# Optimization experiments

Measured on AMD Instinct MI355X. Metric: run time of the kernel, lower is better.

## Reference

```python
import jax, jax.numpy as jnp
import numpy as np

B, N, H, NH = 2, 2048, 1024, 16
DH = H // NH  # 64
SCALE = H ** (-0.5)  # NOTE: original scales by hidden_size**-0.5, not head_dim**-0.5


def setup_inputs() -> dict:
    key = jax.random.key(0)
    k1, k2 = jax.random.split(key)
    hidden_states = jax.random.normal(k1, (B, N, H), dtype=jnp.float32)
    attention_mask = jnp.ones((B, N), dtype=jnp.int32)
    W_qkv = jax.random.normal(k2, (3 * H, H), dtype=jnp.float32) * (H ** -0.5)
    return {"hidden_states": hidden_states, "attention_mask": attention_mask, "W_qkv": W_qkv}


def reference(hidden_states, attention_mask, W_qkv):
    b, n, _ = hidden_states.shape
    # qkv: [b, n, 3H] = x @ W^T  (torch Linear, bias=False)
    qkv = jnp.einsum('bnd,ed->bne', hidden_states, W_qkv)
    # 'b n (k h d) -> k b h n d'
    qkv = qkv.reshape(b, n, 3, NH, DH)
    q, k, v = jnp.moveaxis(qkv, 2, 0).transpose(0, 1, 3, 2, 4)  # each [b, h, n, d]
    scores = jnp.einsum('bhid,bhjd->bhij', q, k) * SCALE
    # mask-fill: attention_mask[:, None, :, None] == 0 -> masks query rows (faithful)
    mask = (attention_mask[:, None, :, None] == 0)
    scores = jnp.where(mask, jnp.asarray(-10000.0, scores.dtype), scores)
    attn = jax.nn.softmax(scores, axis=-1)
    out = jnp.einsum('bhij,bhjd->bhid', attn, v)
    # 'b h n d -> b n (h d)'
    return out.transpose(0, 2, 1, 3).reshape(b, n, NH * DH)
```

## Files before the change

### kernel.cpp

```cpp
#include <hip/hip_runtime.h>
#include <hip/hip_bf16.h>
#include <stdint.h>

#define B_ 2
#define N_ 2048
#define H_ 1024
#define NH_ 16
#define DH_ 64
#define E_ 3072
#define M_ 4096
#define K_ 1024
#define QSCALE2_ 0.0450842200277786f
#define THR2_    11.5415603f

typedef unsigned short ushort_t;
typedef short bf16x8 __attribute__((ext_vector_type(8)));
typedef float f32x4 __attribute__((ext_vector_type(4)));
typedef ushort_t ushort8 __attribute__((ext_vector_type(8)));
typedef ushort_t ushort4v __attribute__((ext_vector_type(4)));
typedef float float4v __attribute__((ext_vector_type(4)));

static __device__ __forceinline__ ushort_t f2bf(float f) {
  __hip_bfloat16 h = __float2bfloat16(f);
  ushort_t u;
  __builtin_memcpy(&u, &h, sizeof(u));
  return u;
}
static __device__ __forceinline__ uint32_t pk2bf(float lo, float hi) {
  return (uint32_t)f2bf(lo) | ((uint32_t)f2bf(hi) << 16);
}
static __device__ __forceinline__ float max3f(float a, float b, float c) {
  return fmaxf(fmaxf(a, b), c);
}

#define GLOAD_LDS16(g, l)                                                   \
  __builtin_amdgcn_global_load_lds(                                         \
      (const __attribute__((address_space(1))) void*)(g),                   \
      (__attribute__((address_space(3))) void*)(l), 16, 0, 0)

__global__ void convert_kernel(const float* __restrict__ X,
                               const float* __restrict__ W,
                               ushort_t* __restrict__ Xb,
                               ushort_t* __restrict__ Wb) {
  const int nx4 = (M_ * K_) / 4;
  int i = blockIdx.x * blockDim.x + threadIdx.x;
  if (i < nx4) {
    float4v v = ((const float4v*)X)[i];
    ushort4v o;
    o[0] = f2bf(v[0]); o[1] = f2bf(v[1]); o[2] = f2bf(v[2]); o[3] = f2bf(v[3]);
    ((ushort4v*)Xb)[i] = o;
  } else {
    int j = i - nx4;
    float4v v = ((const float4v*)W)[j];
    ushort4v o;
    o[0] = f2bf(v[0]); o[1] = f2bf(v[1]); o[2] = f2bf(v[2]); o[3] = f2bf(v[3]);
    ((ushort4v*)Wb)[j] = o;
  }
}

__global__ void gemm_qkv(const ushort_t* __restrict__ Xb,
                         const ushort_t* __restrict__ Wb,
                         ushort_t* __restrict__ Qw,
                         ushort_t* __restrict__ Kw,
                         ushort_t* __restrict__ VTw) {
  __shared__ ushort_t lds_a[128 * 64];
  __shared__ ushort_t lds_b[128 * 64];
  const int tid = threadIdx.x;
  const int lane = tid & 63;
  const int w = tid >> 6;
  const int g = lane >> 4;
  const int l15 = lane & 15;
  const int wid = blockIdx.x;
  const int logical = (wid & 7) * 96 + (wid >> 3);
  const int m0 = (logical / 24) * 128;
  const int e0 = (logical % 24) * 128;
  const int wr = w >> 1, wc = w & 1;

  f32x4 zero = {0.f, 0.f, 0.f, 0.f};
  f32x4 acc[4][4];
#pragma unroll
  for (int mi = 0; mi < 4; ++mi)
#pragma unroll
    for (int ni = 0; ni < 4; ++ni) acc[mi][ni] = zero;

  for (int kt = 0; kt < K_ / 64; ++kt) {
    const int k0 = kt * 64;
#pragma unroll
    for (int i = 0; i < 4; ++i) {
      int chunk = i * 4 + w;
      int c = chunk * 64 + lane;
      int row = c >> 3;
      int col = (c & 7) * 8;
      GLOAD_LDS16(Xb + (size_t)(m0 + row) * K_ + k0 + col, lds_a + chunk * 512);
      GLOAD_LDS16(Wb + (size_t)(e0 + row) * K_ + k0 + col, lds_b + chunk * 512);
    }
    __syncthreads();
#pragma unroll
    for (int ks = 0; ks < 2; ++ks) {
      bf16x8 af[4], bfr[4];
#pragma unroll
      for (int mi = 0; mi < 4; ++mi)
        af[mi] = *(const bf16x8*)(lds_a + (wr * 64 + mi * 16 + l15) * 64 + ks * 32 + g * 8);
#pragma unroll
      for (int ni = 0; ni < 4; ++ni)
        bfr[ni] = *(const bf16x8*)(lds_b + (wc * 64 + ni * 16 + l15) * 64 + ks * 32 + g * 8);
#pragma unroll
      for (int mi = 0; mi < 4; ++mi)
#pragma unroll
        for (int ni = 0; ni < 4; ++ni)
          acc[mi][ni] = __builtin_amdgcn_mfma_f32_16x16x32_bf16(af[mi], bfr[ni], acc[mi][ni], 0, 0, 0);
    }
    __syncthreads();
  }

  const int kidx = e0 >> 10;
  if (kidx == 2) {
#pragma unroll
    for (int ni = 0; ni < 4; ++ni) {
      int e = e0 + wc * 64 + ni * 16 + l15;
      int h = (e >> 6) & 15;
      int d = e & 63;
#pragma unroll
      for (int mi = 0; mi < 4; ++mi) {
        int m = m0 + wr * 64 + mi * 16 + g * 4;
        int b = m >> 11;
        int n = m & (N_ - 1);
        ushort4v pk;
#pragma unroll
        for (int j = 0; j < 4; ++j) pk[j] = f2bf(acc[mi][ni][j]);
        *(ushort4v*)(VTw + ((size_t)(b * NH_ + h) * DH_ + d) * N_ + n) = pk;
      }
    }
  } else {
    ushort_t* dst = (kidx == 0) ? Qw : Kw;
    const float sc = (kidx == 0) ? QSCALE2_ : 1.0f;
#pragma unroll
    for (int ni = 0; ni < 4; ++ni) {
      int e = e0 + wc * 64 + ni * 16 + l15;
      int h = (e >> 6) & 15;
      int d = e & 63;
#pragma unroll
      for (int mi = 0; mi < 4; ++mi) {
#pragma unroll
        for (int j = 0; j < 4; ++j) {
          int m = m0 + wr * 64 + mi * 16 + g * 4 + j;
          int b = m >> 11;
          int n = m & (N_ - 1);
          dst[(size_t)((b * NH_ + h) * N_ + n) * DH_ + d] = f2bf(acc[mi][ni][j] * sc);
        }
      }
    }
  }
}

__global__ __launch_bounds__(128, 1)
void attn_kernel(const ushort_t* __restrict__ Qw,
                 const ushort_t* __restrict__ Kw,
                 const ushort_t* __restrict__ VTw,
                 const int* __restrict__ amask,
                 float* __restrict__ out) {
  __shared__ ushort_t smem[16384 + 9216];
  ushort_t* lds_p = smem + 16384;

  const int tid = threadIdx.x;
  const int lane = tid & 63;
  const int w = tid >> 6;
  const int g = lane >> 4;
  const int l15 = lane & 15;
  const int wid = blockIdx.x;
  const int logical = (wid & 7) * 64 + (wid >> 3);
  const int bh = logical >> 4;
  const int b = bh >> 4, h = bh & 15;
  const int q0 = (logical & 15) * 128;

  const size_t base_nd = (size_t)bh * N_ * DH_;
  const size_t base_dn = (size_t)bh * DH_ * N_;

  const bf16x8 qzero = {0, 0, 0, 0, 0, 0, 0, 0};
  bf16x8 qf[4][2];
#pragma unroll
  for (int qi = 0; qi < 4; ++qi) {
    int q = q0 + w * 64 + qi * 16 + l15;
    int mq = amask[b * N_ + q];
#pragma unroll
    for (int ks = 0; ks < 2; ++ks) {
      bf16x8 v = *(const bf16x8*)(Qw + base_nd + (size_t)q * DH_ + ks * 32 + g * 8);
      qf[qi][ks] = mq ? v : qzero;
    }
  }

  const int st_r = (lane >> 3);
  const int st_s = (lane & 7) ^ st_r;

  f32x4 zero = {0.f, 0.f, 0.f, 0.f};
  f32x4 oacc[4][4];
#pragma unroll
  for (int qi = 0; qi < 4; ++qi)
#pragma unroll
    for (int df = 0; df < 4; ++df) oacc[qi][df] = zero;
  float m_run[4] = {-3.0e38f, -3.0e38f, -3.0e38f, -3.0e38f};
  float l_run[4] = {0.0f, 0.0f, 0.0f, 0.0f};

  const int NT = N_ / 64;

  {
#pragma unroll
    for (int i = 0; i < 4; ++i) {
      int chunk = w * 4 + i;
      int r = chunk * 8 + st_r;
      GLOAD_LDS16(Kw + base_nd + (size_t)r * DH_ + st_s * 8, smem + chunk * 512);
      GLOAD_LDS16(VTw + base_dn + (size_t)r * N_ + st_s * 8, smem + 4096 + chunk * 512);
    }
  }
  __syncthreads();

  for (int it = 0; it < NT; ++it) {
    const int cur = it & 1;
    ushort_t* lk = smem + cur * 8192;
    ushort_t* lv = smem + 4096 + cur * 8192;

    if (it + 1 < NT) {
      const int kv0n = (it + 1) * 64;
      ushort_t* nk = smem + (cur ^ 1) * 8192;
      ushort_t* nv = nk + 4096;
#pragma unroll
      for (int i = 0; i < 4; ++i) {
        int chunk = w * 4 + i;
        int r = chunk * 8 + st_r;
        GLOAD_LDS16(Kw + base_nd + (size_t)(kv0n + r) * DH_ + st_s * 8, nk + chunk * 512);
        GLOAD_LDS16(VTw + base_dn + (size_t)r * N_ + kv0n + st_s * 8, nv + chunk * 512);
      }
    }

    f32x4 sacc[4][4];
#pragma unroll
    for (int qi = 0; qi < 4; ++qi)
#pragma unroll
      for (int kvf = 0; kvf < 4; ++kvf) sacc[qi][kvf] = zero;
    __builtin_amdgcn_s_setprio(1);
#pragma unroll
    for (int ks = 0; ks < 2; ++ks) {
#pragma unroll
      for (int kvf = 0; kvf < 4; ++kvf) {
        bf16x8 a = *(const bf16x8*)(lk + (kvf * 16 + l15) * 64 +
                                    (((ks * 4 + g) ^ (l15 & 7)) * 8));
#pragma unroll
        for (int qi = 0; qi < 4; ++qi)
          sacc[qi][kvf] = __builtin_amdgcn_mfma_f32_16x16x32_bf16(a, qf[qi][ks], sacc[qi][kvf], 0, 0, 0);
      }
    }
    __builtin_amdgcn_s_setprio(0);

    ushort_t* pw = lds_p + w * (64 * 72);
#pragma unroll
    for (int qi = 0; qi < 4; ++qi) {
      float a0 = max3f(sacc[qi][0][0], sacc[qi][0][1], sacc[qi][0][2]);
      float a1 = max3f(sacc[qi][0][3], sacc[qi][1][0], sacc[qi][1][1]);
      float a2 = max3f(sacc[qi][1][2], sacc[qi][1][3], sacc[qi][2][0]);
      float a3 = max3f(sacc[qi][2][1], sacc[qi][2][2], sacc[qi][2][3]);
      float a4 = max3f(sacc[qi][3][0], sacc[qi][3][1], sacc[qi][3][2]);
      float tm = fmaxf(max3f(a0, a1, a2), max3f(a3, a4, sacc[qi][3][3]));
      tm = fmaxf(tm, __shfl_xor(tm, 16));
      tm = fmaxf(tm, __shfl_xor(tm, 32));

      if (__any(tm > m_run[qi] + THR2_)) {
        float m_new = fmaxf(m_run[qi], tm);
        float alpha = exp2f(m_run[qi] - m_new);
        l_run[qi] *= alpha;
#pragma unroll
        for (int df = 0; df < 4; ++df)
#pragma unroll
          for (int j = 0; j < 4; ++j) oacc[qi][df][j] *= alpha;
        m_run[qi] = m_new;
      }

      float p[16];
#pragma unroll
      for (int kvf = 0; kvf < 4; ++kvf)
#pragma unroll
        for (int j = 0; j < 4; ++j)
          p[kvf * 4 + j] = exp2f(sacc[qi][kvf][j] - m_run[qi]);
      float t0 = (p[0] + p[1]) + (p[2] + p[3]);
      float t1 = (p[4] + p[5]) + (p[6] + p[7]);
      float t2 = (p[8] + p[9]) + (p[10] + p[11]);
      float t3 = (p[12] + p[13]) + (p[14] + p[15]);
      float ps = (t0 + t1) + (t2 + t3);
      ps += __shfl_xor(ps, 16);
      ps += __shfl_xor(ps, 32);
      l_run[qi] += ps;

#pragma unroll
      for (int kvf = 0; kvf < 4; ++kvf) {
#pragma unroll
        for (int jj = 0; jj < 2; ++jj) {
          *(uint32_t*)(pw + (qi * 16 + l15) * 72 + kvf * 16 + g * 4 + jj * 2) =
              pk2bf(p[kvf * 4 + jj * 2], p[kvf * 4 + jj * 2 + 1]);
        }
      }
    }

    __builtin_amdgcn_s_setprio(1);
#pragma unroll
    for (int ks = 0; ks < 2; ++ks) {
      bf16x8 pb[4];
#pragma unroll
      for (int qi = 0; qi < 4; ++qi)
        pb[qi] = *(const bf16x8*)(pw + (qi * 16 + l15) * 72 + ks * 32 + g * 8);
#pragma unroll
      for (int df = 0; df < 4; ++df) {
        bf16x8 a = *(const bf16x8*)(lv + (df * 16 + l15) * 64 +
                                    (((ks * 4 + g) ^ (l15 & 7)) * 8));
#pragma unroll
        for (int qi = 0; qi < 4; ++qi)
          oacc[qi][df] = __builtin_amdgcn_mfma_f32_16x16x32_bf16(a, pb[qi], oacc[qi][df], 0, 0, 0);
      }
    }
    __builtin_amdgcn_s_setprio(0);
    __syncthreads();
  }

  float inv[4];
#pragma unroll
  for (int qi = 0; qi < 4; ++qi) inv[qi] = 1.0f / l_run[qi];
  float* osm = (float*)smem;
#pragma unroll
  for (int qi = 0; qi < 4; ++qi)
#pragma unroll
    for (int df = 0; df < 4; ++df)
#pragma unroll
      for (int j = 0; j < 4; ++j)
        osm[(w * 64 + qi * 16 + l15) * 68 + df * 16 + g * 4 + j] = oacc[qi][df][j] * inv[qi];
  __syncthreads();
  int d0 = (tid & 3) * 16;
#pragma unroll
  for (int rr = 0; rr < 4; ++rr) {
    int ql = rr * 32 + (tid >> 2);
    float* dst = out + ((size_t)(b * N_ + q0 + ql)) * H_ + h * DH_ + d0;
#pragma unroll
    for (int jj = 0; jj < 4; ++jj) {
      float4v v;
#pragma unroll
      for (int k = 0; k < 4; ++k) v[k] = osm[ql * 68 + d0 + jj * 4 + k];
      *(float4v*)(dst + jj * 4) = v;
    }
  }
}

extern "C" void kernel_launch(void* const* d_in, const int* in_sizes, int n_in,
                              void* d_out, int out_size, void* d_ws, size_t ws_size,
                              hipStream_t stream) {
  const float* X = (const float*)d_in[0];
  const int* amask = (const int*)d_in[1];
  const float* Wq = (const float*)d_in[2];
  float* out = (float*)d_out;
  char* ws = (char*)d_ws;
  ushort_t* Xb  = (ushort_t*)(ws);
  ushort_t* Wb  = (ushort_t*)(ws + 8388608);
  ushort_t* Qw  = (ushort_t*)(ws + 14680064);
  ushort_t* Kw  = (ushort_t*)(ws + 23068672);
  ushort_t* VTw = (ushort_t*)(ws + 31457280);

  convert_kernel<<<7168, 256, 0, stream>>>(X, Wq, Xb, Wb);
  gemm_qkv<<<768, 256, 0, stream>>>(Xb, Wb, Qw, Kw, VTw);
  attn_kernel<<<512, 128, 0, stream>>>(Qw, Kw, VTw, amask, out);
}
```

Baseline: 222.2 us.

## Split attention query tile across four waves with 32 rows each

The attention block goes from 2 to 4 waves (256 threads), each wave owning 32 query rows instead of 64. K/V tile loads are spread across the four waves, halving per-wave load work. The goal is more waves per CU to hide latency and fewer registers per wave. The trade-off is less reuse of each K/V fragment per MFMA and more barrier participants. P stores also change to 64-bit vector writes.

```diff
diff --git a/kernel.cpp b/kernel.cpp
--- a/kernel.cpp
+++ b/kernel.cpp
@@ -19,6 +19,7 @@
 typedef ushort_t ushort8 __attribute__((ext_vector_type(8)));
 typedef ushort_t ushort4v __attribute__((ext_vector_type(4)));
 typedef float float4v __attribute__((ext_vector_type(4)));
+typedef uint32_t uint2v __attribute__((ext_vector_type(2)));
 
 static __device__ __forceinline__ ushort_t f2bf(float f) {
   __hip_bfloat16 h = __float2bfloat16(f);
@@ -153,7 +154,7 @@
   }
 }
 
-__global__ __launch_bounds__(128, 1)
+__global__ __launch_bounds__(256)
 void attn_kernel(const ushort_t* __restrict__ Qw,
                  const ushort_t* __restrict__ Kw,
                  const ushort_t* __restrict__ VTw,
@@ -177,10 +178,10 @@
   const size_t base_dn = (size_t)bh * DH_ * N_;
 
   const bf16x8 qzero = {0, 0, 0, 0, 0, 0, 0, 0};
-  bf16x8 qf[4][2];
-#pragma unroll
-  for (int qi = 0; qi < 4; ++qi) {
-    int q = q0 + w * 64 + qi * 16 + l15;
+  bf16x8 qf[2][2];
+#pragma unroll
+  for (int qi = 0; qi < 2; ++qi) {
+    int q = q0 + w * 32 + qi * 16 + l15;
     int mq = amask[b * N_ + q];
 #pragma unroll
     for (int ks = 0; ks < 2; ++ks) {
@@ -193,20 +194,20 @@
   const int st_s = (lane & 7) ^ st_r;
 
   f32x4 zero = {0.f, 0.f, 0.f, 0.f};
-  f32x4 oacc[4][4];
-#pragma unroll
-  for (int qi = 0; qi < 4; ++qi)
+  f32x4 oacc[2][4];
+#pragma unroll
+  for (int qi = 0; qi < 2; ++qi)
 #pragma unroll
     for (int df = 0; df < 4; ++df) oacc[qi][df] = zero;
-  float m_run[4] = {-3.0e38f, -3.0e38f, -3.0e38f, -3.0e38f};
-  float l_run[4] = {0.0f, 0.0f, 0.0f, 0.0f};
+  float m_run[2] = {-3.0e38f, -3.0e38f};
+  float l_run[2] = {0.0f, 0.0f};
 
   const int NT = N_ / 64;
 
   {
 #pragma unroll
-    for (int i = 0; i < 4; ++i) {
-      int chunk = w * 4 + i;
+    for (int i = 0; i < 2; ++i) {
+      int chunk = w * 2 + i;
       int r = chunk * 8 + st_r;
       GLOAD_LDS16(Kw + base_nd + (size_t)r * DH_ + st_s * 8, smem + chunk * 512);
       GLOAD_LDS16(VTw + base_dn + (size_t)r * N_ + st_s * 8, smem + 4096 + chunk * 512);
@@ -224,17 +225,17 @@
       ushort_t* nk = smem + (cur ^ 1) * 8192;
       ushort_t* nv = nk + 4096;
 #pragma unroll
-      for (int i = 0; i < 4; ++i) {
-        int chunk = w * 4 + i;
+      for (int i = 0; i < 2; ++i) {
+        int chunk = w * 2 + i;
         int r = chunk * 8 + st_r;
         GLOAD_LDS16(Kw + base_nd + (size_t)(kv0n + r) * DH_ + st_s * 8, nk + chunk * 512);
         GLOAD_LDS16(VTw + base_dn + (size_t)r * N_ + kv0n + st_s * 8, nv + chunk * 512);
       }
     }
 
-    f32x4 sacc[4][4];
-#pragma unroll
-    for (int qi = 0; qi < 4; ++qi)
+    f32x4 sacc[2][4];
+#pragma unroll
+    for (int qi = 0; qi < 2; ++qi)
 #pragma unroll
       for (int kvf = 0; kvf < 4; ++kvf) sacc[qi][kvf] = zero;
     __builtin_amdgcn_s_setprio(1);
@@ -244,16 +245,15 @@
       for (int kvf = 0; kvf < 4; ++kvf) {
         bf16x8 a = *(const bf16x8*)(lk + (kvf * 16 + l15) * 64 +
                                     (((ks * 4 + g) ^ (l15 & 7)) * 8));
-#pragma unroll
-        for (int qi = 0; qi < 4; ++qi)
-          sacc[qi][kvf] = __builtin_amdgcn_mfma_f32_16x16x32_bf16(a, qf[qi][ks], sacc[qi][kvf], 0, 0, 0);
+        sacc[0][kvf] = __builtin_amdgcn_mfma_f32_16x16x32_bf16(a, qf[0][ks], sacc[0][kvf], 0, 0, 0);
+        sacc[1][kvf] = __builtin_amdgcn_mfma_f32_16x16x32_bf16(a, qf[1][ks], sacc[1][kvf], 0, 0, 0);
       }
     }
     __builtin_amdgcn_s_setprio(0);
 
-    ushort_t* pw = lds_p + w * (64 * 72);
-#pragma unroll
-    for (int qi = 0; qi < 4; ++qi) {
+    ushort_t* pw = lds_p + w * (32 * 72);
+#pragma unroll
+    for (int qi = 0; qi < 2; ++qi) {
       float a0 = max3f(sacc[qi][0][0], sacc[qi][0][1], sacc[qi][0][2]);
       float a1 = max3f(sacc[qi][0][3], sacc[qi][1][0], sacc[qi][1][1]);
       float a2 = max3f(sacc[qi][1][2], sacc[qi][1][3], sacc[qi][2][0]);
@@ -291,50 +291,44 @@
 
 #pragma unroll
       for (int kvf = 0; kvf < 4; ++kvf) {
-#pragma unroll
-        for (int jj = 0; jj < 2; ++jj) {
-          *(uint32_t*)(pw + (qi * 16 + l15) * 72 + kvf * 16 + g * 4 + jj * 2) =
-              pk2bf(p[kvf * 4 + jj * 2], p[kvf * 4 + jj * 2 + 1]);
-        }
+        uint2v pkv;
+        pkv[0] = pk2bf(p[kvf * 4 + 0], p[kvf * 4 + 1]);
+        pkv[1] = pk2bf(p[kvf * 4 + 2], p[kvf * 4 + 3]);
+        *(uint2v*)(pw + (qi * 16 + l15) * 72 + kvf * 16 + g * 4) = pkv;
       }
     }
 
     __builtin_amdgcn_s_setprio(1);
 #pragma unroll
     for (int ks = 0; ks < 2; ++ks) {
-      bf16x8 pb[4];
-#pragma unroll
-      for (int qi = 0; qi < 4; ++qi)
-        pb[qi] = *(const bf16x8*)(pw + (qi * 16 + l15) * 72 + ks * 32 + g * 8);
+      bf16x8 pb0 = *(const bf16x8*)(pw + (0 * 16 + l15) * 72 + ks * 32 + g * 8);
+      bf16x8 pb1 = *(const bf16x8*)(pw + (1 * 16 + l15) * 72 + ks * 32 + g * 8);
 #pragma unroll
       for (int df = 0; df < 4; ++df) {
         bf16x8 a = *(const bf16x8*)(lv + (df * 16 + l15) * 64 +
                                     (((ks * 4 + g) ^ (l15 & 7)) * 8));
-#pragma unroll
-        for (int qi = 0; qi < 4; ++qi)
-          oacc[qi][df] = __builtin_amdgcn_mfma_f32_16x16x32_bf16(a, pb[qi], oacc[qi][df], 0, 0, 0);
+        oacc[0][df] = __builtin_amdgcn_mfma_f32_16x16x32_bf16(a, pb0, oacc[0][df], 0, 0, 0);
+        oacc[1][df] = __builtin_amdgcn_mfma_f32_16x16x32_bf16(a, pb1, oacc[1][df], 0, 0, 0);
       }
     }
     __builtin_amdgcn_s_setprio(0);
     __syncthreads();
   }
 
-  float inv[4];
-#pragma unroll
-  for (int qi = 0; qi < 4; ++qi) inv[qi] = 1.0f / l_run[qi];
+  float inv[2] = {1.0f / l_run[0], 1.0f / l_run[1]};
   float* osm = (float*)smem;
 #pragma unroll
-  for (int qi = 0; qi < 4; ++qi)
+  for (int qi = 0; qi < 2; ++qi)
 #pragma unroll
     for (int df = 0; df < 4; ++df)
 #pragma unroll
       for (int j = 0; j < 4; ++j)
-        osm[(w * 64 + qi * 16 + l15) * 68 + df * 16 + g * 4 + j] = oacc[qi][df][j] * inv[qi];
+        osm[(w * 32 + qi * 16 + l15) * 68 + df * 16 + g * 4 + j] = oacc[qi][df][j] * inv[qi];
   __syncthreads();
   int d0 = (tid & 3) * 16;
 #pragma unroll
-  for (int rr = 0; rr < 4; ++rr) {
-    int ql = rr * 32 + (tid >> 2);
+  for (int rr = 0; rr < 2; ++rr) {
+    int ql = rr * 64 + (tid >> 2);
     float* dst = out + ((size_t)(b * N_ + q0 + ql)) * H_ + h * DH_ + d0;
 #pragma unroll
     for (int jj = 0; jj < 4; ++jj) {
@@ -362,5 +356,5 @@
 
   convert_kernel<<<7168, 256, 0, stream>>>(X, Wq, Xb, Wb);
   gemm_qkv<<<768, 256, 0, stream>>>(Xb, Wb, Qw, Kw, VTw);
-  attn_kernel<<<512, 128, 0, stream>>>(Qw, Kw, VTw, amask, out);
-}
+  attn_kernel<<<512, 256, 0, stream>>>(Qw, Kw, VTw, amask, out);
+}
```

After: 195.5 us. 1.14x faster.
